# Kernel tuning notes

Hardware: AMD Instinct MI355X
Metric: run time of the kernel (lower is better)

## Reference

```python
import jax, jax.numpy as jnp
import numpy as np

H = 32        # num_attention_heads
KVH = 8       # num_key_value_heads
D = 2048      # hidden_size
HD = D // H   # head_dim = 64
GROUPS = H // KVH


def setup_inputs() -> dict:
    key = jax.random.key(0)
    k1, k2, k3, k4 = jax.random.split(key, 4)
    B, T = 2, 2048
    x = jax.random.normal(k1, (B, T, D), dtype=jnp.float32)
    wq = jax.random.normal(k2, (D, H * HD), dtype=jnp.float32) * (D ** -0.5)
    wkv = jax.random.normal(k3, (D, 2 * KVH * HD), dtype=jnp.float32) * (D ** -0.5)
    wo = jax.random.normal(k4, (H * HD, D), dtype=jnp.float32) * (D ** -0.5)
    return {"x": x, "wq": wq, "wkv": wkv, "wo": wo}


def reference(x, wq, wkv, wo):
    B, T, _ = x.shape
    scale = HD ** -0.5
    # projections
    q = (x @ wq).reshape(B, T, H, HD).transpose(0, 2, 1, 3)        # [B,H,T,hd]
    kv = x @ wkv                                                    # [B,T,2*KVH*hd]
    k, v = jnp.split(kv, 2, axis=-1)
    k = k.reshape(B, T, KVH, HD).transpose(0, 2, 1, 3)              # [B,KVH,T,hd]
    v = v.reshape(B, T, KVH, HD).transpose(0, 2, 1, 3)
    # repeat_interleave KV heads to match Q heads
    k = jnp.repeat(k, GROUPS, axis=1)                               # [B,H,T,hd]
    v = jnp.repeat(v, GROUPS, axis=1)
    scores = jnp.einsum('bhqd,bhkd->bhqk', q, k) * scale            # [B,H,T,T]
    causal = jnp.triu(jnp.ones((T, T), dtype=bool), k=1)
    scores = jnp.where(causal, -jnp.inf, scores)
    attn = jax.nn.softmax(scores, axis=-1)
    out = jnp.einsum('bhqk,bhkd->bhqd', attn, v)                    # [B,H,T,hd]
    out = out.transpose(0, 2, 1, 3).reshape(B, T, H * HD)
    return out @ wo
```

## Files before the change

### kernel.cpp

```cpp
#include <hip/hip_runtime.h>

using bf16   = __bf16;
using bf16x8 = __attribute__((ext_vector_type(8))) __bf16;
using f32x4  = __attribute__((ext_vector_type(4))) float;

#define T_SEQ 2048
#define NQKV 3072

__device__ __forceinline__ void async_cp16(const bf16* g, bf16* l) {
  __builtin_amdgcn_global_load_lds((__attribute__((address_space(1))) void*)(void*)g,
                                   (__attribute__((address_space(3))) void*)l, 16, 0, 0);
}

__global__ __launch_bounds__(256) void cvt_kernel(const float* __restrict__ in,
                                                  bf16* __restrict__ out) {
  long i = ((long)blockIdx.x * 256 + threadIdx.x) * 8;
  float4 a = *(const float4*)(in + i);
  float4 c = *(const float4*)(in + i + 4);
  bf16x8 v;
  v[0] = (bf16)a.x; v[1] = (bf16)a.y; v[2] = (bf16)a.z; v[3] = (bf16)a.w;
  v[4] = (bf16)c.x; v[5] = (bf16)c.y; v[6] = (bf16)c.z; v[7] = (bf16)c.w;
  *(bf16x8*)(out + i) = v;
}

__global__ __launch_bounds__(256) void transpose_cvt(const float* __restrict__ in,
                                                     bf16* __restrict__ out,
                                                     int R, int C) {
  __shared__ float tile[32][33];
  const int tc = blockIdx.x * 32;
  const int tr = blockIdx.y * 32;
  const int t = threadIdx.x;
  const int lr = t >> 5;
  const int lc = t & 31;
#pragma unroll
  for (int i = 0; i < 4; ++i)
    tile[lr + i * 8][lc] = in[(size_t)(tr + lr + i * 8) * C + tc + lc];
  __syncthreads();
#pragma unroll
  for (int i = 0; i < 4; ++i)
    out[(size_t)(tc + lr + i * 8) * R + tr + lc] = (bf16)tile[lc][lr + i * 8];
}

__global__ __launch_bounds__(256) void transpose_v(const bf16* __restrict__ in,
                                                   bf16* __restrict__ out) {
  __shared__ bf16 tile[32][33];
  const int c0 = blockIdx.x * 32;
  const int r0 = blockIdx.y * 32;
  const int t = threadIdx.x;
  const int lr = t >> 5;
  const int lc = t & 31;
#pragma unroll
  for (int i = 0; i < 4; ++i)
    tile[lr + i * 8][lc] = in[(size_t)(r0 + lr + i * 8) * NQKV + 2560 + c0 + lc];
  __syncthreads();
#pragma unroll
  for (int i = 0; i < 4; ++i) {
    int c = c0 + lr + i * 8;
    int r = r0 + lc;
    out[(size_t)((r >> 11) * 512 + c) * 2048 + (r & 2047)] = tile[lc][lr + i * 8];
  }
}

template <bool OUT_BF16>
__global__ __launch_bounds__(256, 3)
void gemm_kernel(const bf16* __restrict__ A, const bf16* __restrict__ Bt,
                 void* __restrict__ Cout, int Kdim, int Ndim) {
  __shared__ __attribute__((aligned(16))) bf16 As[128 * 64];
  __shared__ __attribute__((aligned(16))) bf16 Bs[128 * 64];
  const int tid  = threadIdx.x;
  const int lane = tid & 63;
  const int wave = tid >> 6;
  const int l16  = lane & 15;
  const int q4   = lane >> 4;
  const long m0 = (long)blockIdx.y * 128;
  const long n0 = (long)blockIdx.x * 128;
  const int wm = (wave >> 1) * 64;
  const int wn = (wave & 1) * 64;

  f32x4 acc[4][4] = {};

  for (int k0 = 0; k0 < Kdim; k0 += 64) {
    __syncthreads();
#pragma unroll
    for (int rr = 0; rr < 4; ++rr) {
      int ci  = rr * 256 + tid;
      int row = ci >> 3;
      int chp = ci & 7;
      int ch  = chp ^ (row & 7);
      async_cp16(A + (m0 + row) * (long)Kdim + k0 + ch * 8, &As[ci * 8]);
      async_cp16(Bt + (n0 + row) * (long)Kdim + k0 + ch * 8, &Bs[ci * 8]);
    }
    __syncthreads();
#pragma unroll
    for (int ks = 0; ks < 2; ++ks) {
      bf16x8 af[4], bfr[4];
#pragma unroll
      for (int mt = 0; mt < 4; ++mt) {
        int row = wm + mt * 16 + l16;
        int chp = (ks * 4 + q4) ^ (row & 7);
        af[mt] = *(const bf16x8*)&As[row * 64 + chp * 8];
      }
#pragma unroll
      for (int nt = 0; nt < 4; ++nt) {
        int row = wn + nt * 16 + l16;
        int chp = (ks * 4 + q4) ^ (row & 7);
        bfr[nt] = *(const bf16x8*)&Bs[row * 64 + chp * 8];
      }
#pragma unroll
      for (int mt = 0; mt < 4; ++mt)
#pragma unroll
        for (int nt = 0; nt < 4; ++nt)
          acc[mt][nt] = __builtin_amdgcn_mfma_f32_16x16x32_bf16(af[mt], bfr[nt],
                                                                acc[mt][nt], 0, 0, 0);
    }
  }
#pragma unroll
  for (int mt = 0; mt < 4; ++mt)
#pragma unroll
    for (int nt = 0; nt < 4; ++nt)
#pragma unroll
      for (int r = 0; r < 4; ++r) {
        long row = m0 + wm + mt * 16 + q4 * 4 + r;
        long col = n0 + wn + nt * 16 + l16;
        float v = acc[mt][nt][r];
        if constexpr (OUT_BF16)
          ((bf16*)Cout)[row * Ndim + col] = (bf16)v;
        else
          ((float*)Cout)[row * Ndim + col] = v;
      }
}

__global__ __launch_bounds__(256, 3)
void attn_kernel(const bf16* __restrict__ qkv, const bf16* __restrict__ vT,
                 bf16* __restrict__ outb) {
  __shared__ __attribute__((aligned(16))) bf16 Ks[64 * 64];
  __shared__ __attribute__((aligned(16))) bf16 Vs[64 * 64];
  __shared__ __attribute__((aligned(16))) bf16 Ps[4][32 * 72];

  const int tid  = threadIdx.x;
  const int lane = tid & 63;
  const int wave = tid >> 6;
  const int l16  = lane & 15;
  const int q4   = lane >> 4;

  const int bid = blockIdx.x;
  const int qt  = 15 - (bid >> 6);
  const int bh  = bid & 63;
  const int b   = bh >> 5;
  const int h   = bh & 31;
  const int kvh = h >> 2;
  const long rowbase = (long)b * T_SEQ;

  const int qrow0 = qt * 128;
  const int wq0   = qrow0 + wave * 32;
  const float cexp = 0.125f * 1.4426950408889634f;

  bf16x8 aq[2][2];
#pragma unroll
  for (int mt = 0; mt < 2; ++mt)
#pragma unroll
    for (int ks = 0; ks < 2; ++ks) {
      bf16x8 v = *(const bf16x8*)(qkv +
          (rowbase + wq0 + mt * 16 + l16) * (long)NQKV + h * 64 + ks * 32 + q4 * 8);
#pragma unroll
      for (int i = 0; i < 8; ++i) v[i] = (bf16)((float)v[i] * cexp);
      aq[mt][ks] = v;
    }

  bf16x8 ones_f;
#pragma unroll
  for (int i = 0; i < 8; ++i) ones_f[i] = (l16 == 0) ? (bf16)1.0f : (bf16)0.0f;

  f32x4 o[2][4] = {};
  f32x4 o_l[2] = {};

  const bf16* kbase = qkv + rowbase * (long)NQKV + 2048 + kvh * 64;
  const bf16* vbase = vT + ((long)b * 512 + kvh * 64) * 2048;

  for (int j0 = 0; j0 < qrow0 + 128; j0 += 64) {
    __syncthreads();
    {
#pragma unroll
      for (int h2 = 0; h2 < 2; ++h2) {
        int ci  = h2 * 256 + tid;
        int row = ci >> 3;
        int ch  = (ci & 7) ^ (row & 7);
        *(bf16x8*)&Ks[ci * 8] =
            *(const bf16x8*)(kbase + (long)(j0 + row) * NQKV + ch * 8);
        *(bf16x8*)&Vs[ci * 8] =
            *(const bf16x8*)(vbase + (long)row * 2048 + j0 + ch * 8);
      }
    }
    __syncthreads();
    if (j0 > wq0 + 31) continue;

    f32x4 s[2][4] = {};
#pragma unroll
    for (int ks = 0; ks < 2; ++ks) {
      bf16x8 bk[4];
#pragma unroll
      for (int nt = 0; nt < 4; ++nt) {
        int row  = nt * 16 + l16;
        int slot = (ks * 4 + q4) ^ (row & 7);
        bk[nt] = *(const bf16x8*)&Ks[row * 64 + slot * 8];
      }
#pragma unroll
      for (int mt = 0; mt < 2; ++mt)
#pragma unroll
        for (int nt = 0; nt < 4; ++nt)
          s[mt][nt] = __builtin_amdgcn_mfma_f32_16x16x32_bf16(aq[mt][ks], bk[nt],
                                                              s[mt][nt], 0, 0, 0);
    }

    if (j0 + 63 > wq0) {
#pragma unroll
      for (int mt = 0; mt < 2; ++mt)
#pragma unroll
        for (int nt = 0; nt < 4; ++nt)
#pragma unroll
          for (int r = 0; r < 4; ++r) {
            int rg = wq0 + mt * 16 + q4 * 4 + r;
            int cg = j0 + nt * 16 + l16;
            if (cg > rg) s[mt][nt][r] = -__builtin_inff();
          }
    }

#pragma unroll
    for (int mt = 0; mt < 2; ++mt)
#pragma unroll
      for (int nt = 0; nt < 4; ++nt)
#pragma unroll
        for (int r = 0; r < 4; ++r) {
          float pv = exp2f(s[mt][nt][r]);
          Ps[wave][(mt * 16 + q4 * 4 + r) * 72 + nt * 16 + l16] = (bf16)pv;
        }

#pragma unroll
    for (int ks = 0; ks < 2; ++ks) {
      bf16x8 ap[2], bv[4];
#pragma unroll
      for (int mt = 0; mt < 2; ++mt)
        ap[mt] = *(const bf16x8*)&Ps[wave][(mt * 16 + l16) * 72 + ks * 32 + q4 * 8];
#pragma unroll
      for (int dt = 0; dt < 4; ++dt) {
        int row  = dt * 16 + l16;
        int slot = (ks * 4 + q4) ^ (row & 7);
        bv[dt] = *(const bf16x8*)&Vs[row * 64 + slot * 8];
      }
#pragma unroll
      for (int mt = 0; mt < 2; ++mt) {
#pragma unroll
        for (int dt = 0; dt < 4; ++dt)
          o[mt][dt] = __builtin_amdgcn_mfma_f32_16x16x32_bf16(ap[mt], bv[dt],
                                                              o[mt][dt], 0, 0, 0);
        o_l[mt] = __builtin_amdgcn_mfma_f32_16x16x32_bf16(ap[mt], ones_f,
                                                          o_l[mt], 0, 0, 0);
      }
    }
  }

#pragma unroll
  for (int mt = 0; mt < 2; ++mt) {
    float inv[4];
#pragma unroll
    for (int r = 0; r < 4; ++r) {
      float lsum = __shfl(o_l[mt][r], lane & 48);
      inv[r] = 1.0f / lsum;
    }
#pragma unroll
    for (int dt = 0; dt < 4; ++dt)
#pragma unroll
      for (int r = 0; r < 4; ++r) {
        long row = rowbase + wq0 + mt * 16 + q4 * 4 + r;
        int col = h * 64 + dt * 16 + l16;
        outb[row * 2048 + col] = (bf16)(o[mt][dt][r] * inv[r]);
      }
  }
}

extern "C" void kernel_launch(void* const* d_in, const int* in_sizes, int n_in,
                              void* d_out, int out_size, void* d_ws, size_t ws_size,
                              hipStream_t stream) {
  const float* x   = (const float*)d_in[0];
  const float* wq  = (const float*)d_in[1];
  const float* wkv = (const float*)d_in[2];
  const float* wo  = (const float*)d_in[3];
  float* out = (float*)d_out;
  char* ws = (char*)d_ws;

  bf16* xbf  = (bf16*)(ws + 0);
  bf16* w1   = (bf16*)(ws + 16777216);
  bf16* qkv  = (bf16*)(ws + 29360128);
  bf16* attn = xbf;
  bf16* vT   = w1;

  const size_t need_parallel = 54525952u + 8388608u;
  bf16* woT;
  bool woT_early;
  if (ws_size >= need_parallel) {
    woT = (bf16*)(ws + 54525952);
    woT_early = true;
  } else {
    woT = qkv;
    woT_early = false;
  }

  cvt_kernel<<<4096, 256, 0, stream>>>(x, xbf);
  transpose_cvt<<<dim3(64, 64), 256, 0, stream>>>(wq, w1, 2048, 2048);
  transpose_cvt<<<dim3(32, 64), 256, 0, stream>>>(wkv, w1 + 2048L * 2048, 2048, 1024);
  if (woT_early)
    transpose_cvt<<<dim3(64, 64), 256, 0, stream>>>(wo, woT, 2048, 2048);

  gemm_kernel<true><<<dim3(24, 32), 256, 0, stream>>>(xbf, w1, (void*)qkv, 2048, 3072);

  transpose_v<<<dim3(16, 128), 256, 0, stream>>>(qkv, vT);

  attn_kernel<<<1024, 256, 0, stream>>>(qkv, vT, attn);

  if (!woT_early)
    transpose_cvt<<<dim3(64, 64), 256, 0, stream>>>(wo, woT, 2048, 2048);

  gemm_kernel<false><<<dim3(16, 32), 256, 0, stream>>>(attn, woT, (void*)out, 2048, 2048);
}
```

Measured before the change: 277.9 us.

## Keep softmax probabilities in registers via transposed QK MFMA and permlane swaps

Swaps the MFMA operands so S is computed transposed, which puts each lane's scores along the key dimension. The probabilities are then packed to bf16 with v_cvt_pk_bf16_f32 and rearranged with permlane16/32 swaps into the A-operand layout for the PV MFMA. This removes the per-wave LDS staging buffer for P along with its write/read round trip. The freed LDS lets launch bounds rise to 4 blocks per CU, at the risk of register pressure and spills.

After: 326.9 us. 1.18x slower.

```diff
diff --git a/kernel.cpp b/kernel.cpp
--- a/kernel.cpp
+++ b/kernel.cpp
@@ -130,12 +130,11 @@
       }
 }
 
-__global__ __launch_bounds__(256, 3)
+__global__ __launch_bounds__(256, 4)
 void attn_kernel(const bf16* __restrict__ qkv, const bf16* __restrict__ vT,
                  bf16* __restrict__ outb) {
   __shared__ __attribute__((aligned(16))) bf16 Ks[64 * 64];
   __shared__ __attribute__((aligned(16))) bf16 Vs[64 * 64];
-  __shared__ __attribute__((aligned(16))) bf16 Ps[4][32 * 72];
 
   const int tid  = threadIdx.x;
   const int lane = tid & 63;
@@ -208,7 +207,7 @@
       for (int mt = 0; mt < 2; ++mt)
 #pragma unroll
         for (int nt = 0; nt < 4; ++nt)
-          s[mt][nt] = __builtin_amdgcn_mfma_f32_16x16x32_bf16(aq[mt][ks], bk[nt],
+          s[mt][nt] = __builtin_amdgcn_mfma_f32_16x16x32_bf16(bk[nt], aq[mt][ks],
                                                               s[mt][nt], 0, 0, 0);
     }
 
@@ -219,28 +218,49 @@
         for (int nt = 0; nt < 4; ++nt)
 #pragma unroll
           for (int r = 0; r < 4; ++r) {
-            int rg = wq0 + mt * 16 + q4 * 4 + r;
-            int cg = j0 + nt * 16 + l16;
+            int rg = wq0 + mt * 16 + l16;
+            int cg = j0 + nt * 16 + q4 * 4 + r;
             if (cg > rg) s[mt][nt][r] = -__builtin_inff();
           }
     }
 
-#pragma unroll
-    for (int mt = 0; mt < 2; ++mt)
-#pragma unroll
-      for (int nt = 0; nt < 4; ++nt)
-#pragma unroll
-        for (int r = 0; r < 4; ++r) {
-          float pv = exp2f(s[mt][nt][r]);
-          Ps[wave][(mt * 16 + q4 * 4 + r) * 72 + nt * 16 + l16] = (bf16)pv;
+    bf16x8 ap[2][2];
+#pragma unroll
+    for (int mt = 0; mt < 2; ++mt) {
+      unsigned pk[4][2];
+#pragma unroll
+      for (int nt = 0; nt < 4; ++nt) {
+        float p0 = exp2f(s[mt][nt][0]);
+        float p1 = exp2f(s[mt][nt][1]);
+        float p2 = exp2f(s[mt][nt][2]);
+        float p3 = exp2f(s[mt][nt][3]);
+        asm("v_cvt_pk_bf16_f32 %0, %1, %2" : "=v"(pk[nt][0]) : "v"(p0), "v"(p1));
+        asm("v_cvt_pk_bf16_f32 %0, %1, %2" : "=v"(pk[nt][1]) : "v"(p2), "v"(p3));
+      }
+#pragma unroll
+      for (int ks = 0; ks < 2; ++ks) {
+        unsigned w0, w1, w2, w3;
+        {
+          unsigned a = pk[2 * ks][0], bb = pk[2 * ks + 1][0];
+          asm("v_permlane32_swap_b32 %0, %1" : "+v"(a), "+v"(bb));
+          asm("v_permlane16_swap_b32 %0, %1" : "+v"(a), "+v"(bb));
+          w0 = a; w2 = bb;
         }
+        {
+          unsigned a = pk[2 * ks][1], bb = pk[2 * ks + 1][1];
+          asm("v_permlane32_swap_b32 %0, %1" : "+v"(a), "+v"(bb));
+          asm("v_permlane16_swap_b32 %0, %1" : "+v"(a), "+v"(bb));
+          w1 = a; w3 = bb;
+        }
+        union { unsigned u[4]; bf16x8 v; } un;
+        un.u[0] = w0; un.u[1] = w1; un.u[2] = w2; un.u[3] = w3;
+        ap[mt][ks] = un.v;
+      }
+    }
 
 #pragma unroll
     for (int ks = 0; ks < 2; ++ks) {
-      bf16x8 ap[2], bv[4];
-#pragma unroll
-      for (int mt = 0; mt < 2; ++mt)
-        ap[mt] = *(const bf16x8*)&Ps[wave][(mt * 16 + l16) * 72 + ks * 32 + q4 * 8];
+      bf16x8 bv[4];
 #pragma unroll
       for (int dt = 0; dt < 4; ++dt) {
         int row  = dt * 16 + l16;
@@ -251,9 +271,9 @@
       for (int mt = 0; mt < 2; ++mt) {
 #pragma unroll
         for (int dt = 0; dt < 4; ++dt)
-          o[mt][dt] = __builtin_amdgcn_mfma_f32_16x16x32_bf16(ap[mt], bv[dt],
+          o[mt][dt] = __builtin_amdgcn_mfma_f32_16x16x32_bf16(ap[mt][ks], bv[dt],
                                                               o[mt][dt], 0, 0, 0);
-        o_l[mt] = __builtin_amdgcn_mfma_f32_16x16x32_bf16(ap[mt], ones_f,
+        o_l[mt] = __builtin_amdgcn_mfma_f32_16x16x32_bf16(ap[mt][ks], ones_f,
                                                           o_l[mt], 0, 0, 0);
       }
     }
```
